# Kernel tuning notes

Hardware: AMD Instinct MI355X
Metric: run time of the kernel (lower is better)

Reference implementation:

```python
import jax, jax.numpy as jnp
import numpy as np

HIDDEN = 192
NUM_LAYERS = 5
ATOMS_PER_MOL = 8
B = 200000
N = B * ATOMS_PER_MOL
EPS = 1e-5  # torch LayerNorm default


def setup_inputs() -> dict:
    key = jax.random.key(0)
    ks = jax.random.split(key, 12)
    z = jax.random.randint(ks[0], (N,), 1, 104, dtype=jnp.int32)
    pos = jax.random.normal(ks[1], (N, 3), dtype=jnp.float32) * 3.0
    batch = (jnp.arange(N, dtype=jnp.int32) // ATOMS_PER_MOL)  # sorted, 8 atoms/molecule
    emb = jax.random.normal(ks[2], (104, HIDDEN), dtype=jnp.float32) * 0.02
    layer_W = jax.random.normal(ks[3], (NUM_LAYERS, HIDDEN, HIDDEN), dtype=jnp.float32) * 0.05
    layer_b = jnp.zeros((NUM_LAYERS, HIDDEN), dtype=jnp.float32)
    layer_g = jnp.ones((NUM_LAYERS, HIDDEN), dtype=jnp.float32)
    layer_beta = jnp.zeros((NUM_LAYERS, HIDDEN), dtype=jnp.float32)
    dist_W = jax.random.normal(ks[4], (HIDDEN, 1), dtype=jnp.float32) * 0.05
    dist_b = jnp.zeros((HIDDEN,), dtype=jnp.float32)
    head_W1 = jax.random.normal(ks[5], (HIDDEN, 3 * HIDDEN), dtype=jnp.float32) * 0.05
    head_b1 = jnp.zeros((HIDDEN,), dtype=jnp.float32)
    head_W2 = jax.random.normal(ks[6], (1, HIDDEN), dtype=jnp.float32) * 0.05
    head_b2 = jnp.zeros((1,), dtype=jnp.float32)
    images = jnp.zeros((1,), dtype=jnp.float32)  # ignored by the model
    return {
        "images": images, "z": z, "pos": pos, "batch": batch,
        "num_molecules": B,
        "emb": emb, "layer_W": layer_W, "layer_b": layer_b,
        "layer_g": layer_g, "layer_beta": layer_beta,
        "dist_W": dist_W, "dist_b": dist_b,
        "head_W1": head_W1, "head_b1": head_b1,
        "head_W2": head_W2, "head_b2": head_b2,
    }


def _layer_norm(y, g, b):
    mu = y.mean(-1, keepdims=True)
    var = y.var(-1, keepdims=True)  # biased, matches torch LayerNorm
    return (y - mu) * jax.lax.rsqrt(var + EPS) * g + b


def _tower(h, layer_W, layer_b, layer_g, layer_beta):
    # residual: h = h + Dropout(ReLU(LN(Linear(h)))); dropout = identity (eval)
    for i in range(layer_W.shape[0]):
        y = h @ layer_W[i].T + layer_b[i]
        h = h + jax.nn.relu(_layer_norm(y, layer_g[i], layer_beta[i]))
    return h


def reference(images, z, pos, batch, num_molecules, emb, layer_W, layer_b,
              layer_g, layer_beta, dist_W, dist_b, head_W1, head_b1,
              head_W2, head_b2):
    Bm = int(num_molecules)
    mol_ids = jnp.arange(Bm, dtype=batch.dtype)
    # batch is sorted -> first atom index of each molecule
    first = jnp.searchsorted(batch, mol_ids)
    counts = jax.ops.segment_sum(jnp.ones_like(batch), batch, num_segments=Bm)
    has2 = counts > 1
    second = jnp.where(has2, first + 1, first)

    h1 = emb[z[first]]   # [B, H]
    h2 = emb[z[second]]  # [B, H]
    h1 = _tower(h1, layer_W, layer_b, layer_g, layer_beta)
    h2 = _tower(h2, layer_W, layer_b, layer_g, layer_beta)

    diff = pos[first] - pos[second]
    dist = jnp.sqrt(jnp.sum(diff * diff, axis=-1) + 1e-12)  # [B]
    dist = jnp.where(has2, dist, 0.0)
    dist_feat = dist[:, None] * dist_W[:, 0][None, :] + dist_b  # Linear(1, H)

    combined = jnp.concatenate([h1, h2, dist_feat], axis=-1)  # [B, 3H]
    x = jax.nn.relu(combined @ head_W1.T + head_b1)
    out = x @ head_W2.T + head_b2  # [B, 1]
    return out.squeeze(-1)
```

## Files before the change

### kernel.cpp

```cpp
#include <hip/hip_runtime.h>

#define H 192
#define NLAYERS 5
#define NTYPES 104
#define EPSLN 1e-5f
#define ATOMS 8
#define MOLBLK 512
#define MOLGRID 256

__device__ __forceinline__ float block_sum_3waves(float v, volatile float* red, int tid) {
  #pragma unroll
  for (int o = 32; o > 0; o >>= 1) v += __shfl_xor(v, o, 64);
  if ((tid & 63) == 0) red[tid >> 6] = v;
  __syncthreads();
  float s = red[0] + red[1] + red[2];
  __syncthreads();
  return s;
}

__global__ __launch_bounds__(192, 1) void build_tables_kernel(
    const float* __restrict__ emb, const float* __restrict__ layer_W,
    const float* __restrict__ layer_b, const float* __restrict__ layer_g,
    const float* __restrict__ layer_beta, const float* __restrict__ dist_W,
    const float* __restrict__ dist_b, const float* __restrict__ head_W1,
    const float* __restrict__ head_b1,
    float* __restrict__ U1, float* __restrict__ U2,
    float* __restrict__ cvec, float* __restrict__ dvec) {
  __shared__ __align__(16) float h[H];
  __shared__ float red[4];
  const int t = blockIdx.x;
  const int j = threadIdx.x;

  h[j] = emb[t * H + j];
  __syncthreads();

  const float4* h4 = reinterpret_cast<const float4*>(h);

  for (int L = 0; L < NLAYERS; ++L) {
    const float4* W4 = reinterpret_cast<const float4*>(layer_W + (L * H + j) * H);
    float acc = layer_b[L * H + j];
    #pragma unroll
    for (int k = 0; k < H / 4; ++k) {
      float4 hv = h4[k];
      float4 wv = W4[k];
      acc = fmaf(hv.x, wv.x, acc);
      acc = fmaf(hv.y, wv.y, acc);
      acc = fmaf(hv.z, wv.z, acc);
      acc = fmaf(hv.w, wv.w, acc);
    }
    float mu = block_sum_3waves(acc, red, j) * (1.0f / H);
    float dev = acc - mu;
    float var = block_sum_3waves(dev * dev, red, j) * (1.0f / H);
    float ln = dev * rsqrtf(var + EPSLN) * layer_g[L * H + j] + layer_beta[L * H + j];
    float hn = h[j] + fmaxf(ln, 0.0f);
    __syncthreads();
    h[j] = hn;
    __syncthreads();
  }

  const float4* w1a = reinterpret_cast<const float4*>(head_W1 + j * (3 * H));
  const float4* w1b = reinterpret_cast<const float4*>(head_W1 + j * (3 * H) + H);
  float a1 = 0.0f, a2 = 0.0f;
  #pragma unroll
  for (int k = 0; k < H / 4; ++k) {
    float4 hv = h4[k];
    float4 va = w1a[k];
    float4 vb = w1b[k];
    a1 = fmaf(hv.x, va.x, a1); a1 = fmaf(hv.y, va.y, a1);
    a1 = fmaf(hv.z, va.z, a1); a1 = fmaf(hv.w, va.w, a1);
    a2 = fmaf(hv.x, vb.x, a2); a2 = fmaf(hv.y, vb.y, a2);
    a2 = fmaf(hv.z, vb.z, a2); a2 = fmaf(hv.w, vb.w, a2);
  }
  U1[t * H + j] = a1;
  U2[t * H + j] = a2;

  if (t == 0) {
    const float4* w1c = reinterpret_cast<const float4*>(head_W1 + j * (3 * H) + 2 * H);
    const float4* dw4 = reinterpret_cast<const float4*>(dist_W);
    const float4* db4 = reinterpret_cast<const float4*>(dist_b);
    float cc = 0.0f, dd = head_b1[j];
    #pragma unroll
    for (int k = 0; k < H / 4; ++k) {
      float4 vc = w1c[k];
      float4 vw = dw4[k];
      float4 vb = db4[k];
      cc = fmaf(vw.x, vc.x, cc); cc = fmaf(vw.y, vc.y, cc);
      cc = fmaf(vw.z, vc.z, cc); cc = fmaf(vw.w, vc.w, cc);
      dd = fmaf(vb.x, vc.x, dd); dd = fmaf(vb.y, vc.y, dd);
      dd = fmaf(vb.z, vc.z, dd); dd = fmaf(vb.w, vc.w, dd);
    }
    cvec[j] = cc;
    dvec[j] = dd;
  }
}

__global__ __launch_bounds__(MOLBLK) void mol_kernel(
    const int* __restrict__ z, const float* __restrict__ pos,
    const float* __restrict__ U1 ,
    const float* __restrict__ cvec, const float* __restrict__ dvec,
    const float* __restrict__ head_W2, const float* __restrict__ head_b2,
    float* __restrict__ out, int B) {
  extern __shared__ __align__(16) float uls[];
  const int tid = threadIdx.x;
  const int l   = tid & 31;

  float c0[6], d0[6], w2[6];
  #pragma unroll
  for (int r = 0; r < 6; ++r) {
    const int jj = l + (r << 5);
    c0[r] = cvec[jj];
    d0[r] = dvec[jj];
    w2[r] = head_W2[jj];
  }
  const float b2 = head_b2[0];

  {
    const float4* src = reinterpret_cast<const float4*>(U1);
    float4* dst = reinterpret_cast<float4*>(uls);
    for (int i = tid; i < (2 * NTYPES * H) / 4; i += MOLBLK) dst[i] = src[i];
  }
  __syncthreads();

  const int hw  = (blockIdx.x << 4) | (tid >> 5);
  const int nhw = gridDim.x << 4;

  for (int m = hw; m < B; m += nhw) {
    const int a0 = m << 3;
    const int2 zz  = *reinterpret_cast<const int2*>(z + a0);
    const float4 p0 = *reinterpret_cast<const float4*>(pos + a0 * 3);
    const float2 p1 = *reinterpret_cast<const float2*>(pos + a0 * 3 + 4);
    const float dx = p0.x - p0.w;
    const float dy = p0.y - p1.x;
    const float dz = p0.z - p1.y;
    const float dist = sqrtf(dx * dx + dy * dy + dz * dz + 1e-12f);

    const float* u1 = uls + zz.x * H;
    const float* u2 = uls + (NTYPES * H) + zz.y * H;

    float acc = 0.f;
    #pragma unroll
    for (int r = 0; r < 6; ++r) {
      const int jj = l + (r << 5);
      float x = u1[jj] + u2[jj] + fmaf(dist, c0[r], d0[r]);
      acc = fmaf(fmaxf(x, 0.f), w2[r], acc);
    }
    #pragma unroll
    for (int o = 16; o > 0; o >>= 1) acc += __shfl_xor(acc, o, 64);
    if (l == 0) out[m] = acc + b2;
  }
}

extern "C" void kernel_launch(void* const* d_in, const int* in_sizes, int n_in,
                              void* d_out, int out_size, void* d_ws, size_t ws_size,
                              hipStream_t stream) {
  const int*   z          = (const int*)  d_in[1];
  const float* pos        = (const float*)d_in[2];
  const float* emb        = (const float*)d_in[5];
  const float* layer_W    = (const float*)d_in[6];
  const float* layer_b    = (const float*)d_in[7];
  const float* layer_g    = (const float*)d_in[8];
  const float* layer_beta = (const float*)d_in[9];
  const float* dist_W     = (const float*)d_in[10];
  const float* dist_b     = (const float*)d_in[11];
  const float* head_W1    = (const float*)d_in[12];
  const float* head_b1    = (const float*)d_in[13];
  const float* head_W2    = (const float*)d_in[14];
  const float* head_b2    = (const float*)d_in[15];
  float* out = (float*)d_out;

  const int N = in_sizes[1];
  const int B = N / ATOMS;

  float* ws = (float*)d_ws;
  float* U1   = ws;
  float* U2   = U1 + NTYPES * H;
  float* cvec = U2 + NTYPES * H;
  float* dvec = cvec + H;

  (void)hipFuncSetAttribute(reinterpret_cast<const void*>(mol_kernel),
                            hipFuncAttributeMaxDynamicSharedMemorySize,
                            2 * NTYPES * H * (int)sizeof(float));

  build_tables_kernel<<<NTYPES, H, 0, stream>>>(
      emb, layer_W, layer_b, layer_g, layer_beta, dist_W, dist_b,
      head_W1, head_b1, U1, U2, cvec, dvec);

  mol_kernel<<<MOLGRID, MOLBLK, 2 * NTYPES * H * sizeof(float), stream>>>(
      z, pos, U1, cvec, dvec, head_W2, head_b2, out, B);
}
```

Measured before the change: 181.7 us.

## Stage weight tiles in padded LDS, double the mol block, prefetch next molecule

The table-building kernel now loads each layer's weight matrix, and the head_W1 slices, into a padded shared-memory tile with coalesced float4 loads. Each thread then reads its row from LDS instead of doing strided per-row global reads. The molecule kernel uses 1024-thread blocks, giving 32 half-waves per block, and software-prefetches the next molecule's z and pos values while computing the current one. The aim is to remove uncoalesced weight traffic in the build step and hide global load latency in the main loop, at the cost of about 150KB of LDS in the build kernel and extra registers.

Result: slower. 207.4 us (+14.2%).

```diff
diff --git a/kernel.cpp b/kernel.cpp
--- a/kernel.cpp
+++ b/kernel.cpp
@@ -5,8 +5,10 @@
 #define NTYPES 104
 #define EPSLN 1e-5f
 #define ATOMS 8
-#define MOLBLK 512
+#define MOLBLK 1024
 #define MOLGRID 256
+#define PADF4 49
+#define WLDS_F (H * PADF4 * 4)
 
 __device__ __forceinline__ float block_sum_3waves(float v, volatile float* red, int tid) {
   #pragma unroll
@@ -26,71 +28,88 @@
     const float* __restrict__ head_b1,
     float* __restrict__ U1, float* __restrict__ U2,
     float* __restrict__ cvec, float* __restrict__ dvec) {
-  __shared__ __align__(16) float h[H];
-  __shared__ float red[4];
-  const int t = blockIdx.x;
-  const int j = threadIdx.x;
+  extern __shared__ __align__(16) float dyn[];
+  float* wlds = dyn;
+  float* h    = dyn + WLDS_F;
+  float* dwb  = h + H;
+  volatile float* red = dwb + 2 * H;
+
+  const int t   = blockIdx.x;
+  const int tid = threadIdx.x;
+  const int j   = tid;
+  const int tj  = tid / 48;
+  const int tc  = tid % 48;
+
+  float4* wl4 = reinterpret_cast<float4*>(wlds);
+  const float4* h4 = reinterpret_cast<const float4*>(h);
+
+  auto stage = [&](const float* gbase, int rs4, int c4off) {
+    const float4* g4 = reinterpret_cast<const float4*>(gbase);
+    #pragma unroll
+    for (int i = 0; i < 48; ++i) {
+      const int jj = 4 * i + tj;
+      wl4[jj * PADF4 + tc] = g4[jj * rs4 + c4off + tc];
+    }
+  };
+  auto dot48 = [&]() {
+    const float4* w4 = wl4 + j * PADF4;
+    float s = 0.f;
+    #pragma unroll
+    for (int c = 0; c < 48; ++c) {
+      float4 wv = w4[c], hv = h4[c];
+      s = fmaf(wv.x, hv.x, s); s = fmaf(wv.y, hv.y, s);
+      s = fmaf(wv.z, hv.z, s); s = fmaf(wv.w, hv.w, s);
+    }
+    return s;
+  };
 
   h[j] = emb[t * H + j];
-  __syncthreads();
-
-  const float4* h4 = reinterpret_cast<const float4*>(h);
 
   for (int L = 0; L < NLAYERS; ++L) {
-    const float4* W4 = reinterpret_cast<const float4*>(layer_W + (L * H + j) * H);
-    float acc = layer_b[L * H + j];
-    #pragma unroll
-    for (int k = 0; k < H / 4; ++k) {
-      float4 hv = h4[k];
-      float4 wv = W4[k];
-      acc = fmaf(hv.x, wv.x, acc);
-      acc = fmaf(hv.y, wv.y, acc);
-      acc = fmaf(hv.z, wv.z, acc);
-      acc = fmaf(hv.w, wv.w, acc);
-    }
-    float mu = block_sum_3waves(acc, red, j) * (1.0f / H);
+    __syncthreads();
+    stage(layer_W + L * H * H, 48, 0);
+    __syncthreads();
+    float acc = layer_b[L * H + j] + dot48();
+    float mu  = block_sum_3waves(acc, red, tid) * (1.0f / H);
     float dev = acc - mu;
-    float var = block_sum_3waves(dev * dev, red, j) * (1.0f / H);
-    float ln = dev * rsqrtf(var + EPSLN) * layer_g[L * H + j] + layer_beta[L * H + j];
-    float hn = h[j] + fmaxf(ln, 0.0f);
+    float var = block_sum_3waves(dev * dev, red, tid) * (1.0f / H);
+    float ln  = dev * rsqrtf(var + EPSLN) * layer_g[L * H + j] + layer_beta[L * H + j];
+    float hn  = h[j] + fmaxf(ln, 0.0f);
     __syncthreads();
     h[j] = hn;
-    __syncthreads();
-  }
-
-  const float4* w1a = reinterpret_cast<const float4*>(head_W1 + j * (3 * H));
-  const float4* w1b = reinterpret_cast<const float4*>(head_W1 + j * (3 * H) + H);
-  float a1 = 0.0f, a2 = 0.0f;
-  #pragma unroll
-  for (int k = 0; k < H / 4; ++k) {
-    float4 hv = h4[k];
-    float4 va = w1a[k];
-    float4 vb = w1b[k];
-    a1 = fmaf(hv.x, va.x, a1); a1 = fmaf(hv.y, va.y, a1);
-    a1 = fmaf(hv.z, va.z, a1); a1 = fmaf(hv.w, va.w, a1);
-    a2 = fmaf(hv.x, vb.x, a2); a2 = fmaf(hv.y, vb.y, a2);
-    a2 = fmaf(hv.z, vb.z, a2); a2 = fmaf(hv.w, vb.w, a2);
-  }
+  }
+
+  __syncthreads();
+  stage(head_W1, 144, 0);
+  __syncthreads();
+  const float a1 = dot48();
+  __syncthreads();
+  stage(head_W1, 144, 48);
+  __syncthreads();
+  const float a2 = dot48();
   U1[t * H + j] = a1;
   U2[t * H + j] = a2;
 
   if (t == 0) {
-    const float4* w1c = reinterpret_cast<const float4*>(head_W1 + j * (3 * H) + 2 * H);
-    const float4* dw4 = reinterpret_cast<const float4*>(dist_W);
-    const float4* db4 = reinterpret_cast<const float4*>(dist_b);
-    float cc = 0.0f, dd = head_b1[j];
-    #pragma unroll
-    for (int k = 0; k < H / 4; ++k) {
-      float4 vc = w1c[k];
-      float4 vw = dw4[k];
-      float4 vb = db4[k];
-      cc = fmaf(vw.x, vc.x, cc); cc = fmaf(vw.y, vc.y, cc);
-      cc = fmaf(vw.z, vc.z, cc); cc = fmaf(vw.w, vc.w, cc);
-      dd = fmaf(vb.x, vc.x, dd); dd = fmaf(vb.y, vc.y, dd);
-      dd = fmaf(vb.z, vc.z, dd); dd = fmaf(vb.w, vc.w, dd);
+    __syncthreads();
+    stage(head_W1, 144, 96);
+    dwb[tid]     = dist_W[tid];
+    dwb[H + tid] = dist_b[tid];
+    __syncthreads();
+    const float4* dw4 = reinterpret_cast<const float4*>(dwb);
+    const float4* db4 = reinterpret_cast<const float4*>(dwb + H);
+    const float4* w4  = wl4 + j * PADF4;
+    float cc = 0.f, dd = 0.f;
+    #pragma unroll
+    for (int c = 0; c < 48; ++c) {
+      float4 wv = w4[c], av = dw4[c], bv = db4[c];
+      cc = fmaf(wv.x, av.x, cc); cc = fmaf(wv.y, av.y, cc);
+      cc = fmaf(wv.z, av.z, cc); cc = fmaf(wv.w, av.w, cc);
+      dd = fmaf(wv.x, bv.x, dd); dd = fmaf(wv.y, bv.y, dd);
+      dd = fmaf(wv.z, bv.z, dd); dd = fmaf(wv.w, bv.w, dd);
     }
     cvec[j] = cc;
-    dvec[j] = dd;
+    dvec[j] = dd + head_b1[j];
   }
 }
 
@@ -121,14 +140,32 @@
   }
   __syncthreads();
 
-  const int hw  = (blockIdx.x << 4) | (tid >> 5);
-  const int nhw = gridDim.x << 4;
-
-  for (int m = hw; m < B; m += nhw) {
+  const int hw  = (blockIdx.x << 5) | (tid >> 5);
+  const int nhw = gridDim.x << 5;
+
+  int m = hw;
+  int2 zz = make_int2(0, 0);
+  float4 p0 = make_float4(0.f, 0.f, 0.f, 0.f);
+  float2 p1 = make_float2(0.f, 0.f);
+  if (m < B) {
     const int a0 = m << 3;
-    const int2 zz  = *reinterpret_cast<const int2*>(z + a0);
-    const float4 p0 = *reinterpret_cast<const float4*>(pos + a0 * 3);
-    const float2 p1 = *reinterpret_cast<const float2*>(pos + a0 * 3 + 4);
+    zz = *reinterpret_cast<const int2*>(z + a0);
+    p0 = *reinterpret_cast<const float4*>(pos + a0 * 3);
+    p1 = *reinterpret_cast<const float2*>(pos + a0 * 3 + 4);
+  }
+
+  while (m < B) {
+    const int mn = m + nhw;
+    int2 zzn = make_int2(0, 0);
+    float4 p0n = make_float4(0.f, 0.f, 0.f, 0.f);
+    float2 p1n = make_float2(0.f, 0.f);
+    if (mn < B) {
+      const int an = mn << 3;
+      zzn = *reinterpret_cast<const int2*>(z + an);
+      p0n = *reinterpret_cast<const float4*>(pos + an * 3);
+      p1n = *reinterpret_cast<const float2*>(pos + an * 3 + 4);
+    }
+
     const float dx = p0.x - p0.w;
     const float dy = p0.y - p1.x;
     const float dz = p0.z - p1.y;
@@ -147,6 +184,8 @@
     #pragma unroll
     for (int o = 16; o > 0; o >>= 1) acc += __shfl_xor(acc, o, 64);
     if (l == 0) out[m] = acc + b2;
+
+    zz = zzn; p0 = p0n; p1 = p1n; m = mn;
   }
 }
 
@@ -177,14 +216,18 @@
   float* cvec = U2 + NTYPES * H;
   float* dvec = cvec + H;
 
+  const int buildLds = (WLDS_F + H + 2 * H + 4) * (int)sizeof(float);
+  const int molLds   = 2 * NTYPES * H * (int)sizeof(float);
+
+  (void)hipFuncSetAttribute(reinterpret_cast<const void*>(build_tables_kernel),
+                            hipFuncAttributeMaxDynamicSharedMemorySize, buildLds);
   (void)hipFuncSetAttribute(reinterpret_cast<const void*>(mol_kernel),
-                            hipFuncAttributeMaxDynamicSharedMemorySize,
-                            2 * NTYPES * H * (int)sizeof(float));
-
-  build_tables_kernel<<<NTYPES, H, 0, stream>>>(
+                            hipFuncAttributeMaxDynamicSharedMemorySize, molLds);
+
+  build_tables_kernel<<<NTYPES, H, buildLds, stream>>>(
       emb, layer_W, layer_b, layer_g, layer_beta, dist_W, dist_b,
       head_W1, head_b1, U1, U2, cvec, dvec);
 
-  mol_kernel<<<MOLGRID, MOLBLK, 2 * NTYPES * H * sizeof(float), stream>>>(
+  mol_kernel<<<MOLGRID, MOLBLK, molLds, stream>>>(
       z, pos, U1, cvec, dvec, head_W2, head_b2, out, B);
 }
```
